# Optimization experiments

Hardware: AMD Instinct MI355X
Metric: run time of the kernel (lower is better)

## Reference

```python
import jax, jax.numpy as jnp
import numpy as np

N_USERS = 100000
N_ITEMS = 100000
N_NODES = N_USERS + N_ITEMS
NNZ = 3200000
EMB = 64
HOPS = 3


def setup_inputs() -> dict:
    key = jax.random.key(0)
    ks = jax.random.split(key, 9)
    return {
        "rows": jax.random.randint(ks[0], (NNZ,), 0, N_NODES, dtype=jnp.int32),
        "cols": jax.random.randint(ks[1], (NNZ,), 0, N_NODES, dtype=jnp.int32),
        "vals": jax.random.uniform(ks[2], (NNZ,), dtype=jnp.float32),
        "user_emb": jax.random.normal(ks[3], (N_USERS, EMB), dtype=jnp.float32) * 0.1,
        "item_emb": jax.random.normal(ks[4], (N_ITEMS, EMB), dtype=jnp.float32) * 0.1,
        "W_gc": jax.random.normal(ks[5], (HOPS, EMB, EMB), dtype=jnp.float32) * 0.1,
        "b_gc": jax.random.normal(ks[6], (HOPS, EMB), dtype=jnp.float32) * 0.1,
        "W_bi": jax.random.normal(ks[7], (HOPS, EMB, EMB), dtype=jnp.float32) * 0.1,
        "b_bi": jax.random.normal(ks[8], (HOPS, EMB), dtype=jnp.float32) * 0.1,
    }


def reference(rows, cols, vals, user_emb, item_emb, W_gc, b_gc, W_bi, b_bi):
    # NGCF.gcn with edge_dropout=False, mess_dropout=False.
    n_nodes = user_emb.shape[0] + item_emb.shape[0]
    ego = jnp.concatenate([user_emb, item_emb], axis=0)  # [N, d]
    all_embeddings = [ego]
    for k in range(W_gc.shape[0]):
        # sparse adjacency propagation: side = A_hat @ ego
        msgs = vals[:, None] * ego[cols]                       # [nnz, d]
        side = jax.ops.segment_sum(msgs, rows, num_segments=n_nodes)  # [N, d]
        sum_emb = side @ W_gc[k] + b_gc[k]                     # [N, d]
        bi_emb = (ego * side) @ W_bi[k] + b_bi[k]              # [N, d]
        ego = jax.nn.leaky_relu(sum_emb + bi_emb, negative_slope=0.2)
        nrm = jnp.sqrt(jnp.sum(ego * ego, axis=1, keepdims=True))
        all_embeddings.append(ego / jnp.maximum(nrm, 1e-12))   # F.normalize(p=2, dim=1)
    # [N, hops+1, d]; original splits into users/items — concatenated here
    return jnp.stack(all_embeddings, axis=1)
```

## Files before the change

### kernel.cpp

```cpp
#include <hip/hip_runtime.h>
#include <hip/hip_fp16.h>

#define N_USERS 100000
#define N_ITEMS 100000
#define N_NODES 200000
#define NNZ     3200000
#define EMB     64
#define HOPS    3
#define SLOTS   (HOPS + 1)
#define ROWSTRIDE (SLOTS * EMB)

#define BROWS 1024
#define NBUCK ((N_NODES + BROWS - 1) / BROWS)
#define CAPB  20
#define EPB   2048
#define TILE  64
#define LPAD  33


__global__ __launch_bounds__(256) void init_ego_q(
    const float* __restrict__ user_emb,
    const float* __restrict__ item_emb,
    float* __restrict__ out,
    signed char* __restrict__ ego8, float* __restrict__ esc)
{
    int gid = blockIdx.x * blockDim.x + threadIdx.x;
    int n = gid >> 6;
    int d = gid & 63;
    if (n >= N_NODES) return;
    float v = (n < N_USERS) ? user_emb[(size_t)n * EMB + d]
                            : item_emb[(size_t)(n - N_USERS) * EMB + d];
    out[(size_t)n * ROWSTRIDE + d] = v;

    float mx = fabsf(v);
    #pragma unroll
    for (int o = 32; o > 0; o >>= 1) mx = fmaxf(mx, __shfl_xor(mx, o));
    float inv = (mx > 0.f) ? 127.f / mx : 0.f;
    ego8[(size_t)n * EMB + d] = (signed char)__float2int_rn(v * inv);
    if (d == 0) esc[n] = mx * (1.f / 127.f);
}

__global__ __launch_bounds__(256) void hist_buckets(
    const int* __restrict__ rows, int* __restrict__ bcnt)
{
    __shared__ int h[NBUCK];
    int t = threadIdx.x;
    if (t < NBUCK) h[t] = 0;
    __syncthreads();
    for (int e = blockIdx.x * blockDim.x + t; e < NNZ; e += gridDim.x * blockDim.x)
        atomicAdd(&h[rows[e] >> 10], 1);
    __syncthreads();
    if (t < NBUCK && h[t]) atomicAdd(&bcnt[t], h[t]);
}

__global__ __launch_bounds__(256) void scan196(
    const int* __restrict__ bcnt, int* __restrict__ boff,
    int* __restrict__ gcur, int* __restrict__ off)
{
    __shared__ int sdata[256];
    int t = threadIdx.x;
    int v = (t < NBUCK) ? bcnt[t] : 0;
    sdata[t] = v;
    __syncthreads();
    #pragma unroll
    for (int ofs = 1; ofs < 256; ofs <<= 1) {
        int add = (t >= ofs) ? sdata[t - ofs] : 0;
        __syncthreads();
        sdata[t] += add;
        __syncthreads();
    }
    if (t < NBUCK) {
        int excl = sdata[t] - v;
        boff[t] = excl;
        gcur[t] = excl;
    }
    if (t == NBUCK - 1) boff[NBUCK] = sdata[t];
    if (t == 0) off[N_NODES] = NNZ;
}

__global__ __launch_bounds__(256) void bucketize(
    const int* __restrict__ rows, const int* __restrict__ cols,
    const float* __restrict__ vals,
    int* __restrict__ gcur,
    unsigned int* __restrict__ cvg, unsigned short* __restrict__ rlg)
{
    __shared__ int hist[NBUCK];
    __shared__ int lofs[NBUCK];
    __shared__ int cnt2[NBUCK];
    __shared__ int gbase[NBUCK];
    __shared__ int sscan[256];
    __shared__ unsigned int   stcv[EPB];
    __shared__ unsigned short strl[EPB];
    __shared__ int            sdst[EPB];

    int t = threadIdx.x;

    for (int base = blockIdx.x * EPB; base < NNZ; base += gridDim.x * EPB) {
        int e1 = min(base + EPB, NNZ);
        int cnt = e1 - base;

        if (t < NBUCK) { hist[t] = 0; cnt2[t] = 0; }
        __syncthreads();

        int myb[8];
        unsigned int mycv[8];
        unsigned short myrl[8];
        #pragma unroll
        for (int u = 0; u < 8; ++u) {
            int idx = base + u * 256 + t;
            myb[u] = -1;
            if (idx < e1) {
                int r = rows[idx];
                int c = cols[idx];
                float v = vals[idx];
                myb[u] = r >> 10;
                unsigned int q14 = (unsigned int)(v * 16383.f + 0.5f);
                mycv[u] = ((unsigned int)c << 14) | q14;
                myrl[u] = (unsigned short)(r & 1023);
                atomicAdd(&hist[myb[u]], 1);
            }
        }
        __syncthreads();

        int hv = (t < NBUCK) ? hist[t] : 0;
        sscan[t] = hv;
        __syncthreads();
        #pragma unroll
        for (int o = 1; o < 256; o <<= 1) {
            int add = (t >= o) ? sscan[t - o] : 0;
            __syncthreads();
            sscan[t] += add;
            __syncthreads();
        }
        if (t < NBUCK) {
            lofs[t] = sscan[t] - hv;
            gbase[t] = atomicAdd(&gcur[t], hv);
        }
        __syncthreads();

        #pragma unroll
        for (int u = 0; u < 8; ++u) {
            if (myb[u] >= 0) {
                int rank = atomicAdd(&cnt2[myb[u]], 1);
                int p = lofs[myb[u]] + rank;
                stcv[p] = mycv[u];
                strl[p] = myrl[u];
                sdst[p] = gbase[myb[u]] + rank;
            }
        }
        __syncthreads();

        for (int j = t; j < cnt; j += 256) {
            int dp = sdst[j];
            cvg[dp] = stcv[j];
            rlg[dp] = strl[j];
        }
        __syncthreads();
    }
}

__global__ __launch_bounds__(1024) void csr_bucket(
    const int* __restrict__ boff,
    unsigned int* __restrict__ cv, const unsigned short* __restrict__ rl,
    int* __restrict__ off)
{
    __shared__ int curL[BROWS];
    __shared__ int sWaveSum[16];
    __shared__ int sWaveOff[16];

    int b = blockIdx.x;
    int t = threadIdx.x;
    int s = boff[b];
    int e = boff[b + 1];

    unsigned int  ecv[CAPB];
    unsigned short erl[CAPB];
    #pragma unroll
    for (int i = 0; i < CAPB; ++i) {
        int idx = s + i * 1024 + t;
        if (idx < e) { ecv[i] = cv[idx]; erl[i] = rl[idx]; }
    }

    curL[t] = 0;
    __syncthreads();

    #pragma unroll
    for (int i = 0; i < CAPB; ++i) {
        int idx = s + i * 1024 + t;
        if (idx < e) atomicAdd(&curL[(int)erl[i]], 1);
    }
    __syncthreads();

    int lane = t & 63;
    int wid  = t >> 6;
    int v = curL[t];
    int inc = v;
    #pragma unroll
    for (int o = 1; o < 64; o <<= 1) {
        int up = __shfl_up(inc, o);
        if (lane >= o) inc += up;
    }
    if (lane == 63) sWaveSum[wid] = inc;
    __syncthreads();
    if (t < 16) {
        int w = sWaveSum[t];
        int wi = w;
        #pragma unroll
        for (int o = 1; o < 16; o <<= 1) {
            int up = __shfl_up(wi, o);
            if (t >= o) wi += up;
        }
        sWaveOff[t] = wi - w;
    }
    __syncthreads();
    int excl = inc - v + sWaveOff[wid];

    int row = b * BROWS + t;
    if (row < N_NODES) off[row] = s + excl;
    __syncthreads();
    curL[t] = s + excl;
    __syncthreads();

    #pragma unroll
    for (int i = 0; i < CAPB; ++i) {
        int idx = s + i * 1024 + t;
        if (idx < e) {
            int p = atomicAdd(&curL[(int)erl[i]], 1);
            cv[p] = ecv[i];
        }
    }
}

__global__ __launch_bounds__(256) void scale_edges(
    const uint4* __restrict__ cv4, const float* __restrict__ esc,
    ushort4* __restrict__ wn4)
{
    const float VS = 1.f / 16383.f;
    int i = blockIdx.x * blockDim.x + threadIdx.x;
    if (i >= NNZ / 4) return;
    uint4 c = cv4[i];
    ushort4 w;
    w.x = __half_as_ushort(__float2half((float)(c.x & 16383u) * VS * esc[c.x >> 14]));
    w.y = __half_as_ushort(__float2half((float)(c.y & 16383u) * VS * esc[c.y >> 14]));
    w.z = __half_as_ushort(__float2half((float)(c.z & 16383u) * VS * esc[c.z >> 14]));
    w.w = __half_as_ushort(__float2half((float)(c.w & 16383u) * VS * esc[c.w >> 14]));
    wn4[i] = w;
}

__global__ __launch_bounds__(256, 4) void gather_side(
    const int* __restrict__ off, const unsigned int* __restrict__ cv,
    const unsigned short* __restrict__ wn,
    const signed char* __restrict__ ego8,
    float* __restrict__ out, int k)
{
    unsigned int d = threadIdx.x & 63;
    int gw = (int)((blockIdx.x * (size_t)blockDim.x + threadIdx.x) >> 6);
    int nw = (gridDim.x * blockDim.x) >> 6;

    float* dst = out + (size_t)(k + 1) * EMB;

    for (int n = gw; n < N_NODES; n += nw) {
        int beg = __builtin_amdgcn_readfirstlane(off[n]);
        int end = __builtin_amdgcn_readfirstlane(off[n + 1]);
        float a0 = 0.f, a1 = 0.f, a2 = 0.f, a3 = 0.f;
        int e = beg;
        for (; e + 16 <= end; e += 16) {
            unsigned int c[16];
            unsigned short wb[16];
            #pragma unroll
            for (int u = 0; u < 16; ++u) c[u] = cv[e + u];
            #pragma unroll
            for (int u = 0; u < 16; ++u) wb[u] = wn[e + u];
            float x[16];
            #pragma unroll
            for (int u = 0; u < 16; ++u)
                x[u] = (float)ego8[(c[u] >> 14) * (unsigned)EMB + d];
            #pragma unroll
            for (int u = 0; u < 16; ++u) {
                float w = __half2float(__ushort_as_half(wb[u]));
                if ((u & 3) == 0) a0 = fmaf(w, x[u], a0);
                else if ((u & 3) == 1) a1 = fmaf(w, x[u], a1);
                else if ((u & 3) == 2) a2 = fmaf(w, x[u], a2);
                else a3 = fmaf(w, x[u], a3);
            }
        }
        for (; e < end; ++e) {
            unsigned int cc = cv[e];
            float w = __half2float(__ushort_as_half(wn[e]));
            a0 = fmaf(w, (float)ego8[(cc >> 14) * (unsigned)EMB + d], a0);
        }
        dst[(size_t)n * ROWSTRIDE + d] = (a0 + a1) + (a2 + a3);
    }
}

__global__ __launch_bounds__(256) void transform_v4(
    const float* __restrict__ Wg, const float* __restrict__ bg,
    const float* __restrict__ Wb, const float* __restrict__ bb,
    signed char* __restrict__ ego8, float* __restrict__ esc,
    float* __restrict__ out, int k, int writeNext)
{
    __shared__ float sS [TILE * LPAD];
    __shared__ float sES[TILE * LPAD];
    __shared__ float rsum[4][TILE];
    __shared__ float rmax[4][TILE];

    int t = threadIdx.x;
    int lane = t & 63;
    int dbase = __builtin_amdgcn_readfirstlane((t >> 6) * 16);

    float* slotK1 = out + (size_t)(k + 1) * EMB;
    int node0 = blockIdx.x * TILE;

    float acc[16];
    #pragma unroll
    for (int di = 0; di < 16; ++di) acc[di] = 0.f;

    int f4 = (t & 7) * 4;
    int nn = t >> 3;

    for (int p = 0; p < 2; ++p) {
        #pragma unroll
        for (int rep = 0; rep < 2; ++rep) {
            int n = nn + 32 * rep;
            size_t sbase = (size_t)(node0 + n) * ROWSTRIDE + 32 * p + f4;
            float4 s4 = *(const float4*)(slotK1 + sbase);
            uchar4 e4 = *(const uchar4*)(ego8 + (size_t)(node0 + n) * EMB + 32 * p + f4);
            float scn = esc[node0 + n];
            int lb = n * LPAD + f4;
            sS [lb + 0] = s4.x; sS [lb + 1] = s4.y; sS [lb + 2] = s4.z; sS [lb + 3] = s4.w;
            sES[lb + 0] = (float)(signed char)e4.x * scn * s4.x;
            sES[lb + 1] = (float)(signed char)e4.y * scn * s4.y;
            sES[lb + 2] = (float)(signed char)e4.z * scn * s4.z;
            sES[lb + 3] = (float)(signed char)e4.w * scn * s4.w;
        }
        __syncthreads();

        for (int jj = 0; jj < 32; ++jj) {
            float sv = sS [lane * LPAD + jj];
            float ev = sES[lane * LPAD + jj];
            int j = 32 * p + jj;
            const float* wgrow = Wg + j * EMB + dbase;
            const float* wbrow = Wb + j * EMB + dbase;
            #pragma unroll
            for (int di = 0; di < 16; ++di)
                acc[di] = fmaf(sv, wgrow[di], fmaf(ev, wbrow[di], acc[di]));
        }
        __syncthreads();
    }

    float o[16];
    float ps = 0.f, pm = 0.f;
    #pragma unroll
    for (int di = 0; di < 16; ++di) {
        float v = acc[di] + (bg[dbase + di] + bb[dbase + di]);
        v = (v > 0.f) ? v : 0.2f * v;
        o[di] = v;
        ps = fmaf(v, v, ps);
        pm = fmaxf(pm, fabsf(v));
    }
    int w = t >> 6;
    rsum[w][lane] = ps;
    rmax[w][lane] = pm;
    __syncthreads();
    float tot = rsum[0][lane] + rsum[1][lane] + rsum[2][lane] + rsum[3][lane];
    float mx  = fmaxf(fmaxf(rmax[0][lane], rmax[1][lane]),
                      fmaxf(rmax[2][lane], rmax[3][lane]));
    float scale = 1.f / fmaxf(sqrtf(tot), 1e-12f);

    if (writeNext) {
        float inv = (mx > 0.f) ? 127.f / mx : 0.f;
        unsigned int wd[4];
        #pragma unroll
        for (int q = 0; q < 4; ++q) {
            unsigned int b0 = (unsigned int)(unsigned char)(signed char)__float2int_rn(o[4*q+0] * inv);
            unsigned int b1 = (unsigned int)(unsigned char)(signed char)__float2int_rn(o[4*q+1] * inv);
            unsigned int b2 = (unsigned int)(unsigned char)(signed char)__float2int_rn(o[4*q+2] * inv);
            unsigned int b3 = (unsigned int)(unsigned char)(signed char)__float2int_rn(o[4*q+3] * inv);
            wd[q] = b0 | (b1 << 8) | (b2 << 16) | (b3 << 24);
        }
        uint4 pk; pk.x = wd[0]; pk.y = wd[1]; pk.z = wd[2]; pk.w = wd[3];
        *(uint4*)(ego8 + (size_t)(node0 + lane) * EMB + dbase) = pk;
        if (t < TILE) esc[node0 + lane] = mx * (1.f / 127.f);
    }

    float* dstp = slotK1 + (size_t)(node0 + lane) * ROWSTRIDE + dbase;
    #pragma unroll
    for (int q = 0; q < 4; ++q) {
        float4 o4;
        o4.x = o[4 * q + 0] * scale;
        o4.y = o[4 * q + 1] * scale;
        o4.z = o[4 * q + 2] * scale;
        o4.w = o[4 * q + 3] * scale;
        *(float4*)(dstp + 4 * q) = o4;
    }
}

extern "C" void kernel_launch(void* const* d_in, const int* in_sizes, int n_in,
                              void* d_out, int out_size, void* d_ws, size_t ws_size,
                              hipStream_t stream)
{
    const int*   rows     = (const int*)d_in[0];
    const int*   cols     = (const int*)d_in[1];
    const float* vals     = (const float*)d_in[2];
    const float* user_emb = (const float*)d_in[3];
    const float* item_emb = (const float*)d_in[4];
    const float* W_gc     = (const float*)d_in[5];
    const float* b_gc     = (const float*)d_in[6];
    const float* W_bi     = (const float*)d_in[7];
    const float* b_bi     = (const float*)d_in[8];
    float* out = (float*)d_out;

    signed char* ego8 = (signed char*)d_ws;
    float* esc = (float*)(ego8 + (size_t)N_NODES * EMB);
    int* bcnt = (int*)(esc + N_NODES);
    int* boff = bcnt + NBUCK;
    int* gcur = boff + NBUCK + 1;
    int* off  = gcur + NBUCK;
    unsigned int* cv = (unsigned int*)(off + N_NODES + 1 + 2);
    unsigned short* wn = (unsigned short*)(cv + NNZ);
    unsigned short* rl = wn + NNZ;

    hipMemsetAsync(bcnt, 0, NBUCK * sizeof(int), stream);
    hist_buckets<<<1024, 256, 0, stream>>>(rows, bcnt);
    scan196<<<1, 256, 0, stream>>>(bcnt, boff, gcur, off);
    bucketize<<<512, 256, 0, stream>>>(rows, cols, vals, gcur, cv, rl);
    csr_bucket<<<NBUCK, 1024, 0, stream>>>(boff, cv, rl, off);

    init_ego_q<<<(N_NODES * 64) / 256, 256, 0, stream>>>(
        user_emb, item_emb, out, ego8, esc);

    scale_edges<<<(NNZ / 4 + 255) / 256, 256, 0, stream>>>(
        (const uint4*)cv, esc, (ushort4*)wn);

    for (int k = 0; k < HOPS; ++k) {
        gather_side<<<2048, 256, 0, stream>>>(off, cv, wn, ego8, out, k);
        transform_v4<<<N_NODES / TILE, 256, 0, stream>>>(
            W_gc + (size_t)k * EMB * EMB, b_gc + (size_t)k * EMB,
            W_bi + (size_t)k * EMB * EMB, b_bi + (size_t)k * EMB,
            ego8, esc, out, k, (k < HOPS - 1) ? 1 : 0);
        if (k < HOPS - 1)
            scale_edges<<<(NNZ / 4 + 255) / 256, 256, 0, stream>>>(
                (const uint4*)cv, esc, (ushort4*)wn);
    }
}
```

Measured before the change: 737.8 us.

## Split wavefront into four edge groups with 4-byte int8 gathers in SpMM

Measured after the change: 657.0 us. -10.9%, faster.

```diff
diff --git a/kernel.cpp b/kernel.cpp
--- a/kernel.cpp
+++ b/kernel.cpp
@@ -247,14 +247,52 @@
     wn4[i] = w;
 }
 
+__device__ __forceinline__ void gstep4(
+    const signed char* __restrict__ ego8,
+    unsigned c0, unsigned c1, unsigned c2, unsigned c3,
+    unsigned wlo, unsigned whi, unsigned g, unsigned dq,
+    float& a0, float& a1, float& a2, float& a3)
+{
+    unsigned cs = (g & 2u) ? ((g & 1u) ? c3 : c2) : ((g & 1u) ? c1 : c0);
+    unsigned wd = (g & 2u) ? whi : wlo;
+    unsigned short wh = (g & 1u) ? (unsigned short)(wd >> 16)
+                                 : (unsigned short)(wd & 0xFFFFu);
+    float w = __half2float(__ushort_as_half(wh));
+    uchar4 x4 = *(const uchar4*)(ego8 + (size_t)(cs >> 14) * EMB + dq * 4u);
+    a0 = fmaf(w, (float)(signed char)x4.x, a0);
+    a1 = fmaf(w, (float)(signed char)x4.y, a1);
+    a2 = fmaf(w, (float)(signed char)x4.z, a2);
+    a3 = fmaf(w, (float)(signed char)x4.w, a3);
+}
+
+__device__ __forceinline__ void gstepm(
+    const signed char* __restrict__ ego8,
+    const unsigned int* __restrict__ cv, const unsigned short* __restrict__ wn,
+    int e, int hi, unsigned g, unsigned dq,
+    float& a0, float& a1, float& a2, float& a3)
+{
+    int idx = e + (int)g;
+    int cl = (idx < hi) ? idx : hi - 1;
+    unsigned c = cv[cl];
+    float w = (idx < hi) ? __half2float(__ushort_as_half(wn[cl])) : 0.f;
+    uchar4 x4 = *(const uchar4*)(ego8 + (size_t)(c >> 14) * EMB + dq * 4u);
+    a0 = fmaf(w, (float)(signed char)x4.x, a0);
+    a1 = fmaf(w, (float)(signed char)x4.y, a1);
+    a2 = fmaf(w, (float)(signed char)x4.z, a2);
+    a3 = fmaf(w, (float)(signed char)x4.w, a3);
+}
+
 __global__ __launch_bounds__(256, 4) void gather_side(
     const int* __restrict__ off, const unsigned int* __restrict__ cv,
     const unsigned short* __restrict__ wn,
     const signed char* __restrict__ ego8,
     float* __restrict__ out, int k)
 {
-    unsigned int d = threadIdx.x & 63;
-    int gw = (int)((blockIdx.x * (size_t)blockDim.x + threadIdx.x) >> 6);
+    int t = threadIdx.x;
+    int lane = t & 63;
+    unsigned g  = (unsigned)(lane >> 4);
+    unsigned dq = (unsigned)(lane & 15);
+    int gw = (int)((blockIdx.x * (size_t)blockDim.x + t) >> 6);
     int nw = (gridDim.x * blockDim.x) >> 6;
 
     float* dst = out + (size_t)(k + 1) * EMB;
@@ -264,32 +302,37 @@
         int end = __builtin_amdgcn_readfirstlane(off[n + 1]);
         float a0 = 0.f, a1 = 0.f, a2 = 0.f, a3 = 0.f;
         int e = beg;
+        if (e < end && (e & 3)) {
+            int ea = (e + 3) & ~3;
+            int ub = (ea < end) ? ea : end;
+            gstepm(ego8, cv, wn, e, ub, g, dq, a0, a1, a2, a3);
+            e = ea;
+        }
         for (; e + 16 <= end; e += 16) {
-            unsigned int c[16];
-            unsigned short wb[16];
-            #pragma unroll
-            for (int u = 0; u < 16; ++u) c[u] = cv[e + u];
-            #pragma unroll
-            for (int u = 0; u < 16; ++u) wb[u] = wn[e + u];
-            float x[16];
-            #pragma unroll
-            for (int u = 0; u < 16; ++u)
-                x[u] = (float)ego8[(c[u] >> 14) * (unsigned)EMB + d];
-            #pragma unroll
-            for (int u = 0; u < 16; ++u) {
-                float w = __half2float(__ushort_as_half(wb[u]));
-                if ((u & 3) == 0) a0 = fmaf(w, x[u], a0);
-                else if ((u & 3) == 1) a1 = fmaf(w, x[u], a1);
-                else if ((u & 3) == 2) a2 = fmaf(w, x[u], a2);
-                else a3 = fmaf(w, x[u], a3);
-            }
-        }
-        for (; e < end; ++e) {
-            unsigned int cc = cv[e];
-            float w = __half2float(__ushort_as_half(wn[e]));
-            a0 = fmaf(w, (float)ego8[(cc >> 14) * (unsigned)EMB + d], a0);
-        }
-        dst[(size_t)n * ROWSTRIDE + d] = (a0 + a1) + (a2 + a3);
+            uint4 ca = *(const uint4*)(cv + e);
+            uint4 cb = *(const uint4*)(cv + e + 4);
+            uint4 cc = *(const uint4*)(cv + e + 8);
+            uint4 cd = *(const uint4*)(cv + e + 12);
+            uint2 w0 = *(const uint2*)(wn + e);
+            uint2 w1 = *(const uint2*)(wn + e + 4);
+            uint2 w2 = *(const uint2*)(wn + e + 8);
+            uint2 w3 = *(const uint2*)(wn + e + 12);
+            gstep4(ego8, ca.x, ca.y, ca.z, ca.w, w0.x, w0.y, g, dq, a0, a1, a2, a3);
+            gstep4(ego8, cb.x, cb.y, cb.z, cb.w, w1.x, w1.y, g, dq, a0, a1, a2, a3);
+            gstep4(ego8, cc.x, cc.y, cc.z, cc.w, w2.x, w2.y, g, dq, a0, a1, a2, a3);
+            gstep4(ego8, cd.x, cd.y, cd.z, cd.w, w3.x, w3.y, g, dq, a0, a1, a2, a3);
+        }
+        for (; e < end; e += 4)
+            gstepm(ego8, cv, wn, e, end, g, dq, a0, a1, a2, a3);
+
+        a0 += __shfl_xor(a0, 16); a0 += __shfl_xor(a0, 32);
+        a1 += __shfl_xor(a1, 16); a1 += __shfl_xor(a1, 32);
+        a2 += __shfl_xor(a2, 16); a2 += __shfl_xor(a2, 32);
+        a3 += __shfl_xor(a3, 16); a3 += __shfl_xor(a3, 32);
+        if (g == 0) {
+            float4 o4; o4.x = a0; o4.y = a1; o4.z = a2; o4.w = a3;
+            *(float4*)(dst + (size_t)n * ROWSTRIDE + dq * 4u) = o4;
+        }
     }
 }
 
```
